# Performance work log

Hardware: AMD Instinct MI355X
Metric: run time of the kernel (lower is better)

The kernel has to match this reference:

```python
import jax, jax.numpy as jnp
import numpy as np

N_NODES = 100000
N_EDGES = 1600000
MSG = 16
HID = 16
N_ETYPE = 8
N_CLASSES = 40


def setup_inputs() -> dict:
    key = jax.random.key(0)
    ks = jax.random.split(key, 11)
    return {
        "features": jax.random.normal(ks[0], (N_NODES, HID), dtype=jnp.float32),
        "src": jax.random.randint(ks[1], (N_EDGES,), 0, N_NODES),
        "dst": jax.random.randint(ks[2], (N_EDGES,), 0, N_NODES),
        "etype": jax.random.randint(ks[3], (N_EDGES,), 0, N_ETYPE),
        "edge_matrix": jax.random.normal(ks[4], (N_ETYPE, MSG * HID), dtype=jnp.float32) * 0.1,
        "w_ih": jax.random.normal(ks[5], (3 * HID, MSG), dtype=jnp.float32) * 0.1,
        "w_hh": jax.random.normal(ks[6], (3 * HID, HID), dtype=jnp.float32) * 0.1,
        "b_ih": jax.random.normal(ks[7], (3 * HID,), dtype=jnp.float32) * 0.1,
        "b_hh": jax.random.normal(ks[8], (3 * HID,), dtype=jnp.float32) * 0.1,
        "out_w": jax.random.normal(ks[9], (N_CLASSES, HID), dtype=jnp.float32) * 0.1,
        "out_b": jax.random.normal(ks[10], (N_CLASSES,), dtype=jnp.float32) * 0.1,
    }


def reference(features, src, dst, etype, edge_matrix, w_ih, w_hh, b_ih, b_hh, out_w, out_b):
    n = features.shape[0]
    # message: per-edge [MSG,HID] matrix (gathered by edge type) times src h
    A = edge_matrix[etype].reshape(-1, MSG, HID)          # [E, MSG, HID]
    msg = jnp.einsum('emh,eh->em', A, features[src])      # [E, MSG]
    # reduce: scatter-sum messages onto destination nodes
    m = jax.ops.segment_sum(msg, dst, num_segments=n)     # [N, MSG]
    # apply: one GRU step per node (PyTorch nn.GRU gate math)
    gi = m @ w_ih.T + b_ih                                # [N, 3*HID]
    gh = features @ w_hh.T + b_hh                         # [N, 3*HID]
    i_r, i_z, i_n = jnp.split(gi, 3, axis=-1)
    h_r, h_z, h_n = jnp.split(gh, 3, axis=-1)
    r = jax.nn.sigmoid(i_r + h_r)
    z = jax.nn.sigmoid(i_z + h_z)
    c = jnp.tanh(i_n + r * h_n)
    h = (1.0 - z) * c + z * features                      # [N, HID]
    return h @ out_w.T + out_b                            # [N, N_CLASSES]
```

## Files before the change

kernel.cpp:

```cpp
#include <hip/hip_runtime.h>
#include <math.h>

constexpr int N_NODES   = 100000;
constexpr int N_EDGES   = 1600000;
constexpr int MSG       = 16;
constexpr int HID       = 16;
constexpr int N_ETYPE   = 8;
constexpr int N_CLASSES = 40;

constexpr int CBSIZE   = 256;
constexpr int NBUCKET  = (N_NODES + CBSIZE - 1) / CBSIZE;
constexpr int SBSIZE   = 32;
constexpr int NSUB     = 8;
constexpr int NSB      = NBUCKET * NSUB;
constexpr int EPB      = 4096;
constexpr int NEBLK    = (N_EDGES + EPB - 1) / EPB;
constexpr int REC_CAP  = 5120;
constexpr int FGRID    = 1043;
constexpr int NSLOT    = 2048;
constexpr int A_STRIDE = 260;

__device__ __forceinline__ float sigmoidf_(float x) { return 1.0f / (1.0f + __expf(-x)); }
__device__ __forceinline__ float tanhf_(float x) { float e = __expf(2.0f * x); return 1.0f - 2.0f / (e + 1.0f); }

__device__ __forceinline__ unsigned f2bf(float f) {
    unsigned u = __float_as_uint(f);
    return (u + 0x7FFFu + ((u >> 16) & 1u)) >> 16;
}
__device__ __forceinline__ float bflo(unsigned u) { return __uint_as_float(u << 16); }
__device__ __forceinline__ float bfhi(unsigned u) { return __uint_as_float(u & 0xFFFF0000u); }

__global__ void __launch_bounds__(256) cvt_kernel(const float* __restrict__ features,
                                                  uint4* __restrict__ featb,
                                                  int* __restrict__ gcursor) {
    int i = blockIdx.x * 256 + threadIdx.x;
    if (i < NBUCKET) gcursor[i] = i * REC_CAP;
    if (i * 8 >= N_NODES * HID) return;
    const float4* fp = reinterpret_cast<const float4*>(features + i * 8);
    float4 a = fp[0], b = fp[1];
    uint4 o;
    o.x = f2bf(a.x) | (f2bf(a.y) << 16);
    o.y = f2bf(a.z) | (f2bf(a.w) << 16);
    o.z = f2bf(b.x) | (f2bf(b.y) << 16);
    o.w = f2bf(b.z) | (f2bf(b.w) << 16);
    featb[i] = o;
}

__global__ void __launch_bounds__(512) partition_kernel(
    const int* __restrict__ src,
    const int* __restrict__ dst,
    const int* __restrict__ etype,
    int* __restrict__ gcursor,
    int* __restrict__ records)
{
    __shared__ int srec[EPB];
    __shared__ unsigned short sbkt[EPB];
    __shared__ int lh[NBUCKET];
    __shared__ int lscan[NBUCKET];
    __shared__ int lofs[NBUCKET];
    __shared__ int gbarr[NBUCKET];
    __shared__ int sscan[512];

    int t = threadIdx.x;
    int base = blockIdx.x * EPB;

    for (int i = t; i < NBUCKET; i += 512) lh[i] = 0;
    __syncthreads();

    int rr[8]; int bb[8];
    #pragma unroll
    for (int q = 0; q < 8; ++q) {
        int e = base + t + 512 * q;
        if (e < N_EDGES) {
            int d = dst[e];
            bb[q] = d >> 8;
            rr[q] = (src[e] << 11) | (etype[e] << 8) | (d & 255);
            atomicAdd(&lh[bb[q]], 1);
        } else bb[q] = -1;
    }
    __syncthreads();

    int i0 = t * 4;
    int v0 = 0, v1 = 0, v2 = 0, v3 = 0;
    if (i0     < NBUCKET) v0 = lh[i0];
    if (i0 + 1 < NBUCKET) v1 = lh[i0 + 1];
    if (i0 + 2 < NBUCKET) v2 = lh[i0 + 2];
    if (i0 + 3 < NBUCKET) v3 = lh[i0 + 3];
    int tsum = v0 + v1 + v2 + v3;
    sscan[t] = tsum;
    __syncthreads();
    for (int off = 1; off < 512; off <<= 1) {
        int tmp = (t >= off) ? sscan[t - off] : 0;
        __syncthreads();
        sscan[t] += tmp;
        __syncthreads();
    }
    int excl = sscan[t] - tsum;
    if (i0     < NBUCKET) { lscan[i0]     = excl; lofs[i0]     = excl; gbarr[i0]     = v0 ? atomicAdd(&gcursor[i0],     v0) : 0; } excl += v0;
    if (i0 + 1 < NBUCKET) { lscan[i0 + 1] = excl; lofs[i0 + 1] = excl; gbarr[i0 + 1] = v1 ? atomicAdd(&gcursor[i0 + 1], v1) : 0; } excl += v1;
    if (i0 + 2 < NBUCKET) { lscan[i0 + 2] = excl; lofs[i0 + 2] = excl; gbarr[i0 + 2] = v2 ? atomicAdd(&gcursor[i0 + 2], v2) : 0; } excl += v2;
    if (i0 + 3 < NBUCKET) { lscan[i0 + 3] = excl; lofs[i0 + 3] = excl; gbarr[i0 + 3] = v3 ? atomicAdd(&gcursor[i0 + 3], v3) : 0; }
    __syncthreads();

    #pragma unroll
    for (int q = 0; q < 8; ++q) {
        if (bb[q] >= 0) {
            int sidx = atomicAdd(&lofs[bb[q]], 1);
            srec[sidx] = rr[q];
            sbkt[sidx] = (unsigned short)bb[q];
        }
    }
    __syncthreads();

    int cnt = min(EPB, N_EDGES - base);
    for (int s2 = t; s2 < cnt; s2 += 512) {
        int b2 = sbkt[s2];
        int pos = gbarr[b2] + (s2 - lscan[b2]);
        if (pos < (b2 + 1) * REC_CAP)
            records[pos] = srec[s2];
    }
}

__global__ void __launch_bounds__(256) partition2_kernel(
    const int* __restrict__ gcursor,
    const int* __restrict__ records,
    int* __restrict__ records2,
    int* __restrict__ slot_off)
{
    __shared__ int hist[NSLOT];
    __shared__ int sscan[256];
    __shared__ int srec[REC_CAP];

    int cb = blockIdx.x;
    int beg = cb * REC_CAP;
    int cnt = min(gcursor[cb] - beg, REC_CAP);
    int t = threadIdx.x;

    #pragma unroll
    for (int j = 0; j < 8; ++j) hist[t * 8 + j] = 0;
    __syncthreads();

    for (int i = t; i < cnt; i += 256) {
        int r = records[beg + i];
        atomicAdd(&hist[((r & 255) << 3) | ((r >> 8) & 7)], 1);
    }
    __syncthreads();

    int loc[8]; int tsum = 0;
    #pragma unroll
    for (int j = 0; j < 8; ++j) { loc[j] = hist[t * 8 + j]; tsum += loc[j]; }
    sscan[t] = tsum;
    __syncthreads();
    for (int off = 1; off < 256; off <<= 1) {
        int tmp = (t >= off) ? sscan[t - off] : 0;
        __syncthreads();
        sscan[t] += tmp;
        __syncthreads();
    }
    int excl = sscan[t] - tsum;
    #pragma unroll
    for (int j = 0; j < 8; ++j) {
        slot_off[cb * (NSLOT + 1) + t * 8 + j] = beg + excl;
        hist[t * 8 + j] = excl;
        excl += loc[j];
    }
    if (t == 0) slot_off[cb * (NSLOT + 1) + NSLOT] = beg + cnt;
    __syncthreads();

    for (int i = t; i < cnt; i += 256) {
        int r = records[beg + i];
        int pos = atomicAdd(&hist[((r & 255) << 3) | ((r >> 8) & 7)], 1);
        srec[pos] = r;
    }
    __syncthreads();
    for (int i = t; i < cnt; i += 256) records2[beg + i] = srec[i];
}

__global__ void __launch_bounds__(256, 4) fused_kernel(
    const uint4* __restrict__ featb,
    const float* __restrict__ features,
    const int*   __restrict__ slot_off,
    const int*   __restrict__ records2,
    const float* __restrict__ edge_matrix,
    const float* __restrict__ w_ih,
    const float* __restrict__ w_hh,
    const float* __restrict__ b_ih,
    const float* __restrict__ b_hh,
    const float* __restrict__ out_w,
    const float* __restrict__ out_b,
    float*       __restrict__ out)
{
    __shared__ float A[N_ETYPE * A_STRIDE];
    __shared__ float hnT[HID][SBSIZE + 1];
    __shared__ float outS[SBSIZE * 44];
    __shared__ float wihL[3 * HID * 17];
    __shared__ float whhL[3 * HID * 17];
    __shared__ float outwL[N_CLASSES * 17];
    __shared__ float bihL[3 * HID];
    __shared__ float bhhL[3 * HID];
    __shared__ float outbL[N_CLASSES];

    int t = threadIdx.x;
    int dl = t >> 3, q = t & 7;
    const float4* feat4 = reinterpret_cast<const float4*>(features);

    for (int i = t; i < N_ETYPE * MSG * HID; i += 256)
        A[(i >> 8) * A_STRIDE + (i & 255)] = edge_matrix[i];
    for (int i = t; i < 3 * HID * MSG; i += 256) wihL[(i >> 4) * 17 + (i & 15)] = w_ih[i];
    for (int i = t; i < 3 * HID * HID; i += 256) whhL[(i >> 4) * 17 + (i & 15)] = w_hh[i];
    for (int i = t; i < N_CLASSES * HID; i += 256) outwL[(i >> 4) * 17 + (i & 15)] = out_w[i];
    if (t < 48) bihL[t] = b_ih[t];
    else if (t < 96) bhhL[t - 48] = b_hh[t - 48];
    else if (t < 136) outbL[t - 96] = out_b[t - 96];

    for (int b = blockIdx.x; b < NSB; b += FGRID) {
        int nodeBase = b * SBSIZE;
        if (nodeBase >= N_NODES) continue;
        int cb = b >> 3, sb = b & 7;
        __syncthreads();

        int go = cb * (NSLOT + 1) + sb * 256 + t;
        int begin = slot_off[go], end = slot_off[go + 1];

        float acc[16];
        #pragma unroll
        for (int k = 0; k < 16; ++k) acc[k] = 0.0f;
        for (int i = begin; i < end; ++i) {
            int rec = records2[i];
            int sn = rec >> 11;
            uint4 ua = featb[2 * sn], ub = featb[2 * sn + 1];
            acc[0]  += bflo(ua.x); acc[1]  += bfhi(ua.x);
            acc[2]  += bflo(ua.y); acc[3]  += bfhi(ua.y);
            acc[4]  += bflo(ua.z); acc[5]  += bfhi(ua.z);
            acc[6]  += bflo(ua.w); acc[7]  += bfhi(ua.w);
            acc[8]  += bflo(ub.x); acc[9]  += bfhi(ub.x);
            acc[10] += bflo(ub.y); acc[11] += bfhi(ub.y);
            acc[12] += bflo(ub.z); acc[13] += bfhi(ub.z);
            acc[14] += bflo(ub.w); acc[15] += bfhi(ub.w);
        }

        float p[16];
        {
            const float* Aq = &A[q * A_STRIDE];
            #pragma unroll
            for (int mm = 0; mm < 16; ++mm) {
                const float4* Ar = reinterpret_cast<const float4*>(Aq + mm * 16);
                float4 x0 = Ar[0], x1 = Ar[1], x2 = Ar[2], x3 = Ar[3];
                p[mm] = x0.x*acc[0]  + x0.y*acc[1]  + x0.z*acc[2]  + x0.w*acc[3]
                      + x1.x*acc[4]  + x1.y*acc[5]  + x1.z*acc[6]  + x1.w*acc[7]
                      + x2.x*acc[8]  + x2.y*acc[9]  + x2.z*acc[10] + x2.w*acc[11]
                      + x3.x*acc[12] + x3.y*acc[13] + x3.z*acc[14] + x3.w*acc[15];
            }
        }
        #pragma unroll
        for (int mm = 0; mm < 16; ++mm) {
            p[mm] += __shfl_xor(p[mm], 1, 64);
            p[mm] += __shfl_xor(p[mm], 2, 64);
            p[mm] += __shfl_xor(p[mm], 4, 64);
        }

        int n = nodeBase + dl;
        float hva[16];
        {
            const float4* hp = feat4 + (size_t)n * 4;
            float4 h0 = hp[0], h1 = hp[1], h2 = hp[2], h3 = hp[3];
            hva[0]=h0.x; hva[1]=h0.y; hva[2]=h0.z; hva[3]=h0.w;
            hva[4]=h1.x; hva[5]=h1.y; hva[6]=h1.z; hva[7]=h1.w;
            hva[8]=h2.x; hva[9]=h2.y; hva[10]=h2.z; hva[11]=h2.w;
            hva[12]=h3.x; hva[13]=h3.y; hva[14]=h3.z; hva[15]=h3.w;
        }
        #pragma unroll
        for (int jj = 0; jj < 2; ++jj) {
            int j = 2 * q + jj;
            float ir  = bihL[j];
            float iz  = bihL[j + HID];
            float inn = bihL[j + 2 * HID];
            float hr  = bhhL[j];
            float hz  = bhhL[j + HID];
            float hnn = bhhL[j + 2 * HID];
            const float* wir = &wihL[j * 17];
            const float* wiz = &wihL[(j + HID) * 17];
            const float* win = &wihL[(j + 2 * HID) * 17];
            const float* whr = &whhL[j * 17];
            const float* whz = &whhL[(j + HID) * 17];
            const float* whn = &whhL[(j + 2 * HID) * 17];
            #pragma unroll
            for (int k = 0; k < HID; ++k) {
                ir  += wir[k] * p[k];
                iz  += wiz[k] * p[k];
                inn += win[k] * p[k];
                hr  += whr[k] * hva[k];
                hz  += whz[k] * hva[k];
                hnn += whn[k] * hva[k];
            }
            float rg = sigmoidf_(ir + hr);
            float zg = sigmoidf_(iz + hz);
            float cg = tanhf_(inn + rg * hnn);
            hnT[j][dl] = (1.0f - zg) * cg + zg * hva[j];
        }
        __syncthreads();

        {
            float hh[HID];
            #pragma unroll
            for (int k = 0; k < HID; ++k) hh[k] = hnT[k][dl];
            #pragma unroll
            for (int cc = 0; cc < 5; ++cc) {
                int c = 5 * q + cc;
                float a2 = outbL[c];
                const float* wr = &outwL[c * 17];
                #pragma unroll
                for (int k = 0; k < HID; ++k) a2 += wr[k] * hh[k];
                outS[dl * 44 + c] = a2;
            }
        }
        __syncthreads();

        {
            float4* ob4 = reinterpret_cast<float4*>(out + (size_t)nodeBase * N_CLASSES);
            #pragma unroll
            for (int rep = 0; rep < 2; ++rep) {
                int i = t + rep * 256;
                if (i < SBSIZE * N_CLASSES / 4) {
                    int node = i / 10, qq = i - node * 10;
                    ob4[i] = *reinterpret_cast<const float4*>(&outS[node * 44 + qq * 4]);
                }
            }
        }
    }
}

extern "C" void kernel_launch(void* const* d_in, const int* in_sizes, int n_in,
                              void* d_out, int out_size, void* d_ws, size_t ws_size,
                              hipStream_t stream) {
    const float* features    = (const float*)d_in[0];
    const int*   src         = (const int*)  d_in[1];
    const int*   dst         = (const int*)  d_in[2];
    const int*   etype       = (const int*)  d_in[3];
    const float* edge_matrix = (const float*)d_in[4];
    const float* w_ih        = (const float*)d_in[5];
    const float* w_hh        = (const float*)d_in[6];
    const float* b_ih        = (const float*)d_in[7];
    const float* b_hh        = (const float*)d_in[8];
    const float* out_w       = (const float*)d_in[9];
    const float* out_b       = (const float*)d_in[10];
    float* out = (float*)d_out;

    int* gcursor  = (int*)d_ws;
    int* slot_off = gcursor + NBUCKET;
    int* records  = slot_off + NBUCKET * (NSLOT + 1);
    int* records2 = records + NBUCKET * REC_CAP;
    size_t featb_off = ((size_t)((char*)(records2 + NBUCKET * REC_CAP) - (char*)d_ws) + 15) & ~15ull;
    uint4* featb = (uint4*)((char*)d_ws + featb_off);

    cvt_kernel<<<(N_NODES * HID / 8 + 255) / 256, 256, 0, stream>>>(features, featb, gcursor);
    partition_kernel<<<NEBLK, 512, 0, stream>>>(src, dst, etype, gcursor, records);
    partition2_kernel<<<NBUCKET, 256, 0, stream>>>(gcursor, records, records2, slot_off);
    fused_kernel<<<FGRID, 256, 0, stream>>>(
        featb, features, slot_off, records2, edge_matrix,
        w_ih, w_hh, b_ih, b_hh, out_w, out_b, out);
}
```

Measured before the change: 125.2 us.

## Make fused kernel wave-independent with shuffle-based hidden exchange, drop block barriers

```diff
diff --git a/kernel.cpp b/kernel.cpp
--- a/kernel.cpp
+++ b/kernel.cpp
@@ -10,15 +10,16 @@
 
 constexpr int CBSIZE   = 256;
 constexpr int NBUCKET  = (N_NODES + CBSIZE - 1) / CBSIZE;
-constexpr int SBSIZE   = 32;
 constexpr int NSUB     = 8;
-constexpr int NSB      = NBUCKET * NSUB;
 constexpr int EPB      = 4096;
 constexpr int NEBLK    = (N_EDGES + EPB - 1) / EPB;
 constexpr int REC_CAP  = 5120;
-constexpr int FGRID    = 1043;
 constexpr int NSLOT    = 2048;
 constexpr int A_STRIDE = 260;
+
+constexpr int NWUNIT   = N_NODES / 8;
+constexpr int FBLK     = 782;
+constexpr int WSTRIDE  = FBLK * 4;
 
 __device__ __forceinline__ float sigmoidf_(float x) { return 1.0f / (1.0f + __expf(-x)); }
 __device__ __forceinline__ float tanhf_(float x) { float e = __expf(2.0f * x); return 1.0f - 2.0f / (e + 1.0f); }
@@ -191,8 +192,6 @@
     float*       __restrict__ out)
 {
     __shared__ float A[N_ETYPE * A_STRIDE];
-    __shared__ float hnT[HID][SBSIZE + 1];
-    __shared__ float outS[SBSIZE * 44];
     __shared__ float wihL[3 * HID * 17];
     __shared__ float whhL[3 * HID * 17];
     __shared__ float outwL[N_CLASSES * 17];
@@ -201,7 +200,8 @@
     __shared__ float outbL[N_CLASSES];
 
     int t = threadIdx.x;
-    int dl = t >> 3, q = t & 7;
+    int lane = t & 63, wid = t >> 6;
+    int dl = lane >> 3, q = lane & 7;
     const float4* feat4 = reinterpret_cast<const float4*>(features);
 
     for (int i = t; i < N_ETYPE * MSG * HID; i += 256)
@@ -212,15 +212,15 @@
     if (t < 48) bihL[t] = b_ih[t];
     else if (t < 96) bhhL[t - 48] = b_hh[t - 48];
     else if (t < 136) outbL[t - 96] = out_b[t - 96];
-
-    for (int b = blockIdx.x; b < NSB; b += FGRID) {
-        int nodeBase = b * SBSIZE;
-        if (nodeBase >= N_NODES) continue;
-        int cb = b >> 3, sb = b & 7;
-        __syncthreads();
-
-        int go = cb * (NSLOT + 1) + sb * 256 + t;
-        int begin = slot_off[go], end = slot_off[go + 1];
+    __syncthreads();
+
+    int gw = blockIdx.x * 4 + wid;
+
+    for (int m = gw; m < NWUNIT; m += WSTRIDE) {
+        int cb = m >> 5;
+        int so = cb * (NSLOT + 1) + (m & 31) * 64;
+        int begin = slot_off[so + lane];
+        int end   = slot_off[so + lane + 1];
 
         float acc[16];
         #pragma unroll
@@ -259,7 +259,7 @@
             p[mm] += __shfl_xor(p[mm], 4, 64);
         }
 
-        int n = nodeBase + dl;
+        int n = m * 8 + dl;
         float hva[16];
         {
             const float4* hp = feat4 + (size_t)n * 4;
@@ -269,6 +269,7 @@
             hva[8]=h2.x; hva[9]=h2.y; hva[10]=h2.z; hva[11]=h2.w;
             hva[12]=h3.x; hva[13]=h3.y; hva[14]=h3.z; hva[15]=h3.w;
         }
+        float hg[2];
         #pragma unroll
         for (int jj = 0; jj < 2; ++jj) {
             int j = 2 * q + jj;
@@ -296,36 +297,27 @@
             float rg = sigmoidf_(ir + hr);
             float zg = sigmoidf_(iz + hz);
             float cg = tanhf_(inn + rg * hnn);
-            hnT[j][dl] = (1.0f - zg) * cg + zg * hva[j];
-        }
-        __syncthreads();
-
-        {
-            float hh[HID];
+            float hj = features[(size_t)n * HID + j];
+            hg[jj] = (1.0f - zg) * cg + zg * hj;
+        }
+
+        int lanebase = lane & 56;
+        float hh[16];
+        #pragma unroll
+        for (int qq = 0; qq < 8; ++qq) {
+            hh[2 * qq]     = __shfl(hg[0], lanebase + qq, 64);
+            hh[2 * qq + 1] = __shfl(hg[1], lanebase + qq, 64);
+        }
+
+        float* op = out + (size_t)n * N_CLASSES + 5 * q;
+        #pragma unroll
+        for (int cc = 0; cc < 5; ++cc) {
+            int c = 5 * q + cc;
+            float a2 = outbL[c];
+            const float* wr = &outwL[c * 17];
             #pragma unroll
-            for (int k = 0; k < HID; ++k) hh[k] = hnT[k][dl];
-            #pragma unroll
-            for (int cc = 0; cc < 5; ++cc) {
-                int c = 5 * q + cc;
-                float a2 = outbL[c];
-                const float* wr = &outwL[c * 17];
-                #pragma unroll
-                for (int k = 0; k < HID; ++k) a2 += wr[k] * hh[k];
-                outS[dl * 44 + c] = a2;
-            }
-        }
-        __syncthreads();
-
-        {
-            float4* ob4 = reinterpret_cast<float4*>(out + (size_t)nodeBase * N_CLASSES);
-            #pragma unroll
-            for (int rep = 0; rep < 2; ++rep) {
-                int i = t + rep * 256;
-                if (i < SBSIZE * N_CLASSES / 4) {
-                    int node = i / 10, qq = i - node * 10;
-                    ob4[i] = *reinterpret_cast<const float4*>(&outS[node * 44 + qq * 4]);
-                }
-            }
+            for (int k = 0; k < HID; ++k) a2 += wr[k] * hh[k];
+            op[cc] = a2;
         }
     }
 }
@@ -356,7 +348,7 @@
     cvt_kernel<<<(N_NODES * HID / 8 + 255) / 256, 256, 0, stream>>>(features, featb, gcursor);
     partition_kernel<<<NEBLK, 512, 0, stream>>>(src, dst, etype, gcursor, records);
     partition2_kernel<<<NBUCKET, 256, 0, stream>>>(gcursor, records, records2, slot_off);
-    fused_kernel<<<FGRID, 256, 0, stream>>>(
+    fused_kernel<<<FBLK, 256, 0, stream>>>(
         featb, features, slot_off, records2, edge_matrix,
         w_ih, w_hh, b_ih, b_hh, out_w, out_b, out);
 }
```

Result: slower. 427.3 us (+241.4%).
